# Kernel tuning notes

Measured on AMD Instinct MI355X. Metric: run time of the kernel, lower is better.

## Reference

```python
import jax, jax.numpy as jnp
import numpy as np
import math

B, S, DIM = 32, 1, 4096
NH, NKV, HD = 32, 8, 128
MAXLEN = 4096
START_POS = 4095


def _rope(t, freqs):
    # t: (b, s, h, hd); freqs: (s, hd//2, 2) = (cos/real, sin/imag)
    b, s, h, hd = t.shape
    tr = t.astype(jnp.float32).reshape(b, s, h, hd // 2, 2)
    c = freqs[None, :, None, :, 0]
    sn = freqs[None, :, None, :, 1]
    x0, x1 = tr[..., 0], tr[..., 1]
    out = jnp.stack([x0 * c - x1 * sn, x0 * sn + x1 * c], axis=-1)
    return out.reshape(b, s, h, hd).astype(t.dtype)


def setup_inputs() -> dict:
    key = jax.random.key(0)
    ks = jax.random.split(key, 8)
    sd = 1.0 / math.sqrt(DIM)
    x = jax.random.normal(ks[0], (B, S, DIM), dtype=jnp.float32)
    freqs = jax.random.normal(ks[1], (S, HD // 2, 2), dtype=jnp.float32)
    cache_k = jax.random.normal(ks[2], (B, MAXLEN, NKV, HD), dtype=jnp.float32)
    cache_v = jax.random.normal(ks[3], (B, MAXLEN, NKV, HD), dtype=jnp.float32)
    wq = jax.random.normal(ks[4], (NH * HD, DIM), dtype=jnp.float32) * sd
    wk = jax.random.normal(ks[5], (NKV * HD, DIM), dtype=jnp.float32) * sd
    wv = jax.random.normal(ks[6], (NKV * HD, DIM), dtype=jnp.float32) * sd
    wo = jax.random.normal(ks[7], (DIM, NH * HD), dtype=jnp.float32) * sd
    return {"x": x, "freqs": freqs, "cache_k": cache_k, "cache_v": cache_v,
            "wq": wq, "wk": wk, "wv": wv, "wo": wo, "start_pos": START_POS}


def reference(x, freqs, cache_k, cache_v, wq, wk, wv, wo, start_pos):
    b, s, _ = x.shape
    n_rep = NH // NKV
    xq = (x @ wq.T).reshape(b, s, NH, HD)
    xk = (x @ wk.T).reshape(b, s, NKV, HD)
    xv = (x @ wv.T).reshape(b, s, NKV, HD)
    xq = _rope(xq, freqs)
    xk = _rope(xk, freqs)
    # KV-cache write then read of prefix (static start_pos)
    keys = cache_k.at[:, start_pos:start_pos + s].set(xk)[:, :start_pos + s]
    values = cache_v.at[:, start_pos:start_pos + s].set(xv)[:, :start_pos + s]
    # GQA: group q heads (g=NKV kv groups, r=n_rep) without materializing repeat
    q = xq.reshape(b, s, NKV, n_rep, HD)
    scores = jnp.einsum('bsgrd,blgd->bgrsl', q, keys) / math.sqrt(HD)
    probs = jax.nn.softmax(scores.astype(jnp.float32), axis=-1).astype(xq.dtype)
    out = jnp.einsum('bgrsl,blgd->bsgrd', probs, values).reshape(b, s, NH * HD)
    return out @ wo.T
```

## Files before the change

kernel.cpp:

```cpp
#include <hip/hip_runtime.h>

#define QSCALE 0.08838834764831845f


#define GEMM_FMA(r, wf) \
    acc[r][0] = fmaf(wf.x, x0.x, acc[r][0]); acc[r][0] = fmaf(wf.y, x0.y, acc[r][0]); \
    acc[r][0] = fmaf(wf.z, x0.z, acc[r][0]); acc[r][0] = fmaf(wf.w, x0.w, acc[r][0]); \
    acc[r][1] = fmaf(wf.x, x1.x, acc[r][1]); acc[r][1] = fmaf(wf.y, x1.y, acc[r][1]); \
    acc[r][1] = fmaf(wf.z, x1.z, acc[r][1]); acc[r][1] = fmaf(wf.w, x1.w, acc[r][1]); \
    acc[r][2] = fmaf(wf.x, x2.x, acc[r][2]); acc[r][2] = fmaf(wf.y, x2.y, acc[r][2]); \
    acc[r][2] = fmaf(wf.z, x2.z, acc[r][2]); acc[r][2] = fmaf(wf.w, x2.w, acc[r][2]); \
    acc[r][3] = fmaf(wf.x, x3.x, acc[r][3]); acc[r][3] = fmaf(wf.y, x3.y, acc[r][3]); \
    acc[r][3] = fmaf(wf.z, x3.z, acc[r][3]); acc[r][3] = fmaf(wf.w, x3.w, acc[r][3]);

__device__ __forceinline__ void gemv3(
    const float* __restrict__ W,
    const float* __restrict__ X,
    float* __restrict__ part, const int M, const int m0, const int ks)
{
    const int t = threadIdx.x;
    const int ksub = t & 3;
    const int ngrp = (t >> 2) & 7;
    const int mgrp = t >> 5;

    const int kbase = ks * 256 + ksub * 4;
    const float* wr0 = W + (size_t)(mgrp * 8 + 0) * 4096 + kbase;
    const float* wr1 = W + (size_t)(mgrp * 8 + 1) * 4096 + kbase;
    const float* wr2 = W + (size_t)(mgrp * 8 + 2) * 4096 + kbase;
    const float* wr3 = W + (size_t)(mgrp * 8 + 3) * 4096 + kbase;
    const float* wr4 = W + (size_t)(mgrp * 8 + 4) * 4096 + kbase;
    const float* wr5 = W + (size_t)(mgrp * 8 + 5) * 4096 + kbase;
    const float* wr6 = W + (size_t)(mgrp * 8 + 6) * 4096 + kbase;
    const float* wr7 = W + (size_t)(mgrp * 8 + 7) * 4096 + kbase;
    const float* xr0 = X + (size_t)(ngrp * 4 + 0) * 4096 + kbase;
    const float* xr1 = X + (size_t)(ngrp * 4 + 1) * 4096 + kbase;
    const float* xr2 = X + (size_t)(ngrp * 4 + 2) * 4096 + kbase;
    const float* xr3 = X + (size_t)(ngrp * 4 + 3) * 4096 + kbase;

    float acc[8][4];
#pragma unroll
    for (int r = 0; r < 8; ++r)
#pragma unroll
        for (int n = 0; n < 4; ++n) acc[r][n] = 0.f;

#pragma unroll 2
    for (int c = 0; c < 16; ++c) {
        const int off = c * 16;
        const float4 w0 = *(const float4*)(wr0 + off);
        const float4 w1 = *(const float4*)(wr1 + off);
        const float4 w2 = *(const float4*)(wr2 + off);
        const float4 w3 = *(const float4*)(wr3 + off);
        const float4 w4 = *(const float4*)(wr4 + off);
        const float4 w5 = *(const float4*)(wr5 + off);
        const float4 w6 = *(const float4*)(wr6 + off);
        const float4 w7 = *(const float4*)(wr7 + off);
        const float4 x0 = *(const float4*)(xr0 + off);
        const float4 x1 = *(const float4*)(xr1 + off);
        const float4 x2 = *(const float4*)(xr2 + off);
        const float4 x3 = *(const float4*)(xr3 + off);
        GEMM_FMA(0, w0) GEMM_FMA(1, w1) GEMM_FMA(2, w2) GEMM_FMA(3, w3)
        GEMM_FMA(4, w4) GEMM_FMA(5, w5) GEMM_FMA(6, w6) GEMM_FMA(7, w7)
    }

#pragma unroll
    for (int r = 0; r < 8; ++r)
#pragma unroll
        for (int n = 0; n < 4; ++n) {
            acc[r][n] += __shfl_xor(acc[r][n], 1);
            acc[r][n] += __shfl_xor(acc[r][n], 2);
        }

    if (ksub == 0) {
        float* base = part + (size_t)ks * 32 * M + m0 + mgrp * 8;
#pragma unroll
        for (int n = 0; n < 4; ++n) {
            float* dst = base + (size_t)(ngrp * 4 + n) * M;
            *(float4*)(dst)     = make_float4(acc[0][n], acc[1][n], acc[2][n], acc[3][n]);
            *(float4*)(dst + 4) = make_float4(acc[4][n], acc[5][n], acc[6][n], acc[7][n]);
        }
    }
}

__global__ __launch_bounds__(256, 4) void gemv_qkv_kernel(
    const float* __restrict__ wq, const float* __restrict__ wk,
    const float* __restrict__ wv, const float* __restrict__ x,
    float* __restrict__ part)
{
    const int mb = blockIdx.x >> 4, ks = blockIdx.x & 15;
    const int m0 = mb * 64;
    const float* W;
    if (m0 < 4096)      W = wq + (size_t)m0 * 4096;
    else if (m0 < 5120) W = wk + (size_t)(m0 - 4096) * 4096;
    else                W = wv + (size_t)(m0 - 5120) * 4096;
    gemv3(W, x, part, 6144, m0, ks);
}

__global__ __launch_bounds__(256, 4) void gemv_out_kernel(
    const float* __restrict__ wo, const float* __restrict__ a_ws,
    float* __restrict__ part)
{
    const int mb = blockIdx.x >> 4, ks = blockIdx.x & 15;
    gemv3(wo + (size_t)(mb * 64) * 4096, a_ws, part, 4096, mb * 64, ks);
}

__global__ __launch_bounds__(256) void qkv_combine_kernel(
    const float* __restrict__ part,
    const float* __restrict__ freqs,
    float* __restrict__ qc_g, float* __restrict__ kn_g, float* __restrict__ vn_g)
{
    const int idx = blockIdx.x * 256 + threadIdx.x;
    const int b = idx / 1536;
    const int cm = (idx - b * 1536) * 4;
    const float* p = part + (size_t)b * 6144 + cm;
    float4 v = make_float4(0.f, 0.f, 0.f, 0.f);
#pragma unroll
    for (int s = 0; s < 16; ++s) {
        const float4 a = *(const float4*)(p + (size_t)s * (32 * 6144));
        v.x += a.x; v.y += a.y; v.z += a.z; v.w += a.w;
    }
    if (cm < 4096) {
        const int d = cm & 127;
        const float4 f = *(const float4*)(freqs + d);
        float4 o;
        o.x = (v.x * f.x - v.y * f.y) * QSCALE;
        o.y = (v.x * f.y + v.y * f.x) * QSCALE;
        o.z = (v.z * f.z - v.w * f.w) * QSCALE;
        o.w = (v.z * f.w + v.w * f.z) * QSCALE;
        *(float4*)(qc_g + (size_t)b * 4096 + cm) = o;
    } else if (cm < 5120) {
        const int d = (cm - 4096) & 127;
        const float4 f = *(const float4*)(freqs + d);
        float4 o;
        o.x = v.x * f.x - v.y * f.y;
        o.y = v.x * f.y + v.y * f.x;
        o.z = v.z * f.z - v.w * f.w;
        o.w = v.z * f.w + v.w * f.z;
        *(float4*)(kn_g + (size_t)b * 1024 + (cm - 4096)) = o;
    } else {
        *(float4*)(vn_g + (size_t)b * 1024 + (cm - 5120)) = v;
    }
}

__global__ __launch_bounds__(256, 4) void attn4_kernel(
    const float* __restrict__ qc_g, const float* __restrict__ kn_g,
    const float* __restrict__ vn_g,
    const float* __restrict__ cache_k, const float* __restrict__ cache_v,
    float* __restrict__ pmss, float* __restrict__ pacc)
{
    const int t = threadIdx.x;
    const int w = t >> 6, lane = t & 63;
    const int g2 = lane >> 5, j = lane & 31;
    const int bid = blockIdx.x;
    const int q2 = bid & 1, split = (bid >> 1) & 15, b = bid >> 5;
    const int gsub = w >> 1, rsub = w & 1;
    const int g = q2 * 4 + gsub * 2 + g2;
    const int row0 = split * 256 + rsub * 128;

    float4 q[4];
    const float* qb = qc_g + (size_t)b * 4096 + (size_t)g * 512 + j * 4;
#pragma unroll
    for (int h = 0; h < 4; ++h) q[h] = *(const float4*)(qb + h * 128);

    float m[4]  = {-1e30f, -1e30f, -1e30f, -1e30f};
    float ss[4] = {0.f, 0.f, 0.f, 0.f};
    float4 acc[4];
#pragma unroll
    for (int h = 0; h < 4; ++h) acc[h] = make_float4(0.f, 0.f, 0.f, 0.f);

    auto process = [&](const float4 kf, const float4 vf) {
        float d[4];
#pragma unroll
        for (int h = 0; h < 4; ++h)
            d[h] = fmaf(q[h].x, kf.x, fmaf(q[h].y, kf.y,
                   fmaf(q[h].z, kf.z, q[h].w * kf.w)));
#pragma unroll
        for (int mask = 1; mask <= 16; mask <<= 1) {
            d[0] += __shfl_xor(d[0], mask);
            d[1] += __shfl_xor(d[1], mask);
            d[2] += __shfl_xor(d[2], mask);
            d[3] += __shfl_xor(d[3], mask);
        }
#pragma unroll
        for (int h = 0; h < 4; ++h) {
            const float dd = d[h] - m[h];
            float pe;
            if (dd > 8.0f) {
                const float c = __expf(-dd);
                ss[h] = fmaf(ss[h], c, 1.0f);
                acc[h].x *= c; acc[h].y *= c; acc[h].z *= c; acc[h].w *= c;
                m[h] = d[h]; pe = 1.0f;
            } else {
                pe = __expf(dd);
                ss[h] += pe;
            }
            acc[h].x = fmaf(pe, vf.x, acc[h].x);
            acc[h].y = fmaf(pe, vf.y, acc[h].y);
            acc[h].z = fmaf(pe, vf.z, acc[h].z);
            acc[h].w = fmaf(pe, vf.w, acc[h].w);
        }
    };

    const size_t cbase = ((size_t)b * 4096 + row0) * 1024 + (size_t)g * 128 + j * 4;
    const float* kp = cache_k + cbase;
    const float* vp = cache_v + cbase;

    const bool lastw = (split == 15) && (rsub == 1);
    const int n = lastw ? 127 : 128;

    float4 kA = *(const float4*)(kp);
    float4 vA = *(const float4*)(vp);
    float4 kB = *(const float4*)(kp + 1024);
    float4 vB = *(const float4*)(vp + 1024);
#pragma unroll 2
    for (int i = 0; i < n; ++i) {
        float4 kC, vC;
        if (i + 2 < n) {
            kC = *(const float4*)(kp + (size_t)(i + 2) * 1024);
            vC = *(const float4*)(vp + (size_t)(i + 2) * 1024);
        }
        process(kA, vA);
        kA = kB; vA = vB; kB = kC; vB = vC;
    }
    if (lastw) {
        const float4 kf = *(const float4*)(kn_g + (size_t)b * 1024 + (size_t)g * 128 + j * 4);
        const float4 vf = *(const float4*)(vn_g + (size_t)b * 1024 + (size_t)g * 128 + j * 4);
        process(kf, vf);
    }

    const int pidx = (((b * 16 + split) * 2 + rsub) * 8 + g) * 4;
#pragma unroll
    for (int h = 0; h < 4; ++h)
        *(float4*)(pacc + (size_t)(pidx + h) * 128 + j * 4) = acc[h];
    if (j == 0) {
#pragma unroll
        for (int h = 0; h < 4; ++h) {
            pmss[(size_t)(pidx + h) * 2]     = m[h];
            pmss[(size_t)(pidx + h) * 2 + 1] = ss[h];
        }
    }
}

__global__ __launch_bounds__(128) void attn_combine_kernel(
    const float* __restrict__ pmss, const float* __restrict__ pacc,
    float* __restrict__ a_ws)
{
    const int bg = blockIdx.x, t = threadIdx.x;
    const int h = t >> 5, jj = t & 31;
    const int b = bg >> 3, g = bg & 7;

    float M = -1e30f;
#pragma unroll
    for (int s = 0; s < 16; ++s)
#pragma unroll
        for (int r = 0; r < 2; ++r) {
            const int idx = (((b * 16 + s) * 2 + r) * 8 + g) * 4 + h;
            M = fmaxf(M, pmss[(size_t)idx * 2]);
        }
    float SS = 0.f;
    float4 o = make_float4(0.f, 0.f, 0.f, 0.f);
#pragma unroll
    for (int s = 0; s < 16; ++s)
#pragma unroll
        for (int r = 0; r < 2; ++r) {
            const int idx = (((b * 16 + s) * 2 + r) * 8 + g) * 4 + h;
            const float wgt = __expf(pmss[(size_t)idx * 2] - M);
            SS = fmaf(pmss[(size_t)idx * 2 + 1], wgt, SS);
            const float4 a = *(const float4*)(pacc + (size_t)idx * 128 + jj * 4);
            o.x = fmaf(a.x, wgt, o.x);
            o.y = fmaf(a.y, wgt, o.y);
            o.z = fmaf(a.z, wgt, o.z);
            o.w = fmaf(a.w, wgt, o.w);
        }
    const float inv = 1.f / SS;
    o.x *= inv; o.y *= inv; o.z *= inv; o.w *= inv;
    *(float4*)(a_ws + (size_t)b * 4096 + (size_t)(g * 4 + h) * 128 + jj * 4) = o;
}

__global__ __launch_bounds__(256) void out_combine_kernel(
    const float* __restrict__ part, float* __restrict__ out)
{
    const int i4 = (blockIdx.x * 256 + threadIdx.x) * 4;
    float4 v = make_float4(0.f, 0.f, 0.f, 0.f);
#pragma unroll
    for (int s = 0; s < 16; ++s) {
        const float4 a = *(const float4*)(part + (size_t)s * 131072 + i4);
        v.x += a.x; v.y += a.y; v.z += a.z; v.w += a.w;
    }
    *(float4*)(out + i4) = v;
}

extern "C" void kernel_launch(void* const* d_in, const int* in_sizes, int n_in,
                              void* d_out, int out_size, void* d_ws, size_t ws_size,
                              hipStream_t stream)
{
    const float* x       = (const float*)d_in[0];
    const float* freqs   = (const float*)d_in[1];
    const float* cache_k = (const float*)d_in[2];
    const float* cache_v = (const float*)d_in[3];
    const float* wq      = (const float*)d_in[4];
    const float* wk      = (const float*)d_in[5];
    const float* wv      = (const float*)d_in[6];
    const float* wo      = (const float*)d_in[7];

    float* out = (float*)d_out;
    float* ws  = (float*)d_ws;
    float* part_qkv = ws;
    float* qc_g     = ws + 3145728;
    float* kn_g     = ws + 3276800;
    float* vn_g     = ws + 3309568;
    float* pmss     = ws + 3342336;
    float* pacc     = ws + 3407872;
    float* a_ws     = ws + 7602176;
    float* part_out = ws + 7733248;

    gemv_qkv_kernel<<<1536, 256, 0, stream>>>(wq, wk, wv, x, part_qkv);
    qkv_combine_kernel<<<192, 256, 0, stream>>>(part_qkv, freqs, qc_g, kn_g, vn_g);
    attn4_kernel<<<1024, 256, 0, stream>>>(qc_g, kn_g, vn_g, cache_k, cache_v, pmss, pacc);
    attn_combine_kernel<<<256, 128, 0, stream>>>(pmss, pacc, a_ws);
    gemv_out_kernel<<<1024, 256, 0, stream>>>(wo, a_ws, part_out);
    out_combine_kernel<<<128, 256, 0, stream>>>(part_out, out);
}
```

Before: 330.8 us.

## Fuse QKV split-K reduction and RoPE into attention kernel, deepen KV prefetch

Removes the separate qkv_combine kernel. Each attention block now reduces the 16 split-K partials for its own q heads and k/v group, applies RoPE and the q scaling, and stages the results in shared memory. This saves one launch and the round trip of q/k/v through global memory. The cost is redundant reduction work, because 16 splits per batch each recompute the same q/k/v. The KV loop is also restructured to prefetch four rows at a time instead of two, to keep more loads in flight.

```diff
diff --git a/kernel.cpp b/kernel.cpp
--- a/kernel.cpp
+++ b/kernel.cpp
@@ -103,47 +103,9 @@
     gemv3(wo + (size_t)(mb * 64) * 4096, a_ws, part, 4096, mb * 64, ks);
 }
 
-__global__ __launch_bounds__(256) void qkv_combine_kernel(
-    const float* __restrict__ part,
+__global__ __launch_bounds__(256, 4) void attn5_kernel(
+    const float* __restrict__ part_qkv,
     const float* __restrict__ freqs,
-    float* __restrict__ qc_g, float* __restrict__ kn_g, float* __restrict__ vn_g)
-{
-    const int idx = blockIdx.x * 256 + threadIdx.x;
-    const int b = idx / 1536;
-    const int cm = (idx - b * 1536) * 4;
-    const float* p = part + (size_t)b * 6144 + cm;
-    float4 v = make_float4(0.f, 0.f, 0.f, 0.f);
-#pragma unroll
-    for (int s = 0; s < 16; ++s) {
-        const float4 a = *(const float4*)(p + (size_t)s * (32 * 6144));
-        v.x += a.x; v.y += a.y; v.z += a.z; v.w += a.w;
-    }
-    if (cm < 4096) {
-        const int d = cm & 127;
-        const float4 f = *(const float4*)(freqs + d);
-        float4 o;
-        o.x = (v.x * f.x - v.y * f.y) * QSCALE;
-        o.y = (v.x * f.y + v.y * f.x) * QSCALE;
-        o.z = (v.z * f.z - v.w * f.w) * QSCALE;
-        o.w = (v.z * f.w + v.w * f.z) * QSCALE;
-        *(float4*)(qc_g + (size_t)b * 4096 + cm) = o;
-    } else if (cm < 5120) {
-        const int d = (cm - 4096) & 127;
-        const float4 f = *(const float4*)(freqs + d);
-        float4 o;
-        o.x = v.x * f.x - v.y * f.y;
-        o.y = v.x * f.y + v.y * f.x;
-        o.z = v.z * f.z - v.w * f.w;
-        o.w = v.z * f.w + v.w * f.z;
-        *(float4*)(kn_g + (size_t)b * 1024 + (cm - 4096)) = o;
-    } else {
-        *(float4*)(vn_g + (size_t)b * 1024 + (cm - 5120)) = v;
-    }
-}
-
-__global__ __launch_bounds__(256, 4) void attn4_kernel(
-    const float* __restrict__ qc_g, const float* __restrict__ kn_g,
-    const float* __restrict__ vn_g,
     const float* __restrict__ cache_k, const float* __restrict__ cache_v,
     float* __restrict__ pmss, float* __restrict__ pacc)
 {
@@ -153,13 +115,65 @@
     const int bid = blockIdx.x;
     const int q2 = bid & 1, split = (bid >> 1) & 15, b = bid >> 5;
     const int gsub = w >> 1, rsub = w & 1;
-    const int g = q2 * 4 + gsub * 2 + g2;
+    const int g  = q2 * 4 + gsub * 2 + g2;
+    const int gl = gsub * 2 + g2;
     const int row0 = split * 256 + rsub * 128;
 
+    __shared__ float qc[16][128];
+    __shared__ float knl[4][128];
+    __shared__ float vnl[4][128];
+
+    const size_t PS = 32 * 6144;
+    {
+        const int H = t >> 4, dq = (t & 15) * 8;
+        const float* p = part_qkv + (size_t)b * 6144 + (size_t)(q2 * 16 + H) * 128 + dq;
+        float4 s0 = make_float4(0.f, 0.f, 0.f, 0.f);
+        float4 s1 = make_float4(0.f, 0.f, 0.f, 0.f);
+#pragma unroll
+        for (int s = 0; s < 16; ++s) {
+            const float4 a = *(const float4*)(p + s * PS);
+            const float4 c = *(const float4*)(p + s * PS + 4);
+            s0.x += a.x; s0.y += a.y; s0.z += a.z; s0.w += a.w;
+            s1.x += c.x; s1.y += c.y; s1.z += c.z; s1.w += c.w;
+        }
+        const float4 f0 = *(const float4*)(freqs + dq);
+        const float4 f1 = *(const float4*)(freqs + dq + 4);
+        qc[H][dq + 0] = (s0.x * f0.x - s0.y * f0.y) * QSCALE;
+        qc[H][dq + 1] = (s0.x * f0.y + s0.y * f0.x) * QSCALE;
+        qc[H][dq + 2] = (s0.z * f0.z - s0.w * f0.w) * QSCALE;
+        qc[H][dq + 3] = (s0.z * f0.w + s0.w * f0.z) * QSCALE;
+        qc[H][dq + 4] = (s1.x * f1.x - s1.y * f1.y) * QSCALE;
+        qc[H][dq + 5] = (s1.x * f1.y + s1.y * f1.x) * QSCALE;
+        qc[H][dq + 6] = (s1.z * f1.z - s1.w * f1.w) * QSCALE;
+        qc[H][dq + 7] = (s1.z * f1.w + s1.w * f1.z) * QSCALE;
+    }
+    {
+        const int tv = t & 127;
+        const int glp = tv >> 5, d4 = (tv & 31) * 4;
+        const int moff = (t < 128 ? 4096 : 5120) + (q2 * 4 + glp) * 128 + d4;
+        const float* p = part_qkv + (size_t)b * 6144 + moff;
+        float4 s0 = make_float4(0.f, 0.f, 0.f, 0.f);
+#pragma unroll
+        for (int s = 0; s < 16; ++s) {
+            const float4 a = *(const float4*)(p + s * PS);
+            s0.x += a.x; s0.y += a.y; s0.z += a.z; s0.w += a.w;
+        }
+        if (t < 128) {
+            const float4 f = *(const float4*)(freqs + d4);
+            knl[glp][d4 + 0] = s0.x * f.x - s0.y * f.y;
+            knl[glp][d4 + 1] = s0.x * f.y + s0.y * f.x;
+            knl[glp][d4 + 2] = s0.z * f.z - s0.w * f.w;
+            knl[glp][d4 + 3] = s0.z * f.w + s0.w * f.z;
+        } else {
+            vnl[glp][d4 + 0] = s0.x; vnl[glp][d4 + 1] = s0.y;
+            vnl[glp][d4 + 2] = s0.z; vnl[glp][d4 + 3] = s0.w;
+        }
+    }
+    __syncthreads();
+
     float4 q[4];
-    const float* qb = qc_g + (size_t)b * 4096 + (size_t)g * 512 + j * 4;
-#pragma unroll
-    for (int h = 0; h < 4; ++h) q[h] = *(const float4*)(qb + h * 128);
+#pragma unroll
+    for (int h = 0; h < 4; ++h) q[h] = *(const float4*)&qc[gl * 4 + h][j * 4];
 
     float m[4]  = {-1e30f, -1e30f, -1e30f, -1e30f};
     float ss[4] = {0.f, 0.f, 0.f, 0.f};
@@ -207,23 +221,40 @@
     const bool lastw = (split == 15) && (rsub == 1);
     const int n = lastw ? 127 : 128;
 
-    float4 kA = *(const float4*)(kp);
-    float4 vA = *(const float4*)(vp);
-    float4 kB = *(const float4*)(kp + 1024);
-    float4 vB = *(const float4*)(vp + 1024);
-#pragma unroll 2
-    for (int i = 0; i < n; ++i) {
-        float4 kC, vC;
-        if (i + 2 < n) {
-            kC = *(const float4*)(kp + (size_t)(i + 2) * 1024);
-            vC = *(const float4*)(vp + (size_t)(i + 2) * 1024);
-        }
+    float4 kA, vA, kB, vB, kC, vC, kD, vD;
+    kA = *(const float4*)(kp);        vA = *(const float4*)(vp);
+    kB = *(const float4*)(kp + 1024); vB = *(const float4*)(vp + 1024);
+    int i = 0;
+    for (; i + 4 <= n; i += 4) {
+        const float* k2 = kp + (size_t)(i + 2) * 1024;
+        const float* v2 = vp + (size_t)(i + 2) * 1024;
+        kC = *(const float4*)(k2);        vC = *(const float4*)(v2);
+        kD = *(const float4*)(k2 + 1024); vD = *(const float4*)(v2 + 1024);
         process(kA, vA);
-        kA = kB; vA = vB; kB = kC; vB = vC;
+        process(kB, vB);
+        if (i + 6 <= n) {
+            const float* k4 = kp + (size_t)(i + 4) * 1024;
+            const float* v4 = vp + (size_t)(i + 4) * 1024;
+            kA = *(const float4*)(k4);        vA = *(const float4*)(v4);
+            kB = *(const float4*)(k4 + 1024); vB = *(const float4*)(v4 + 1024);
+        } else if (i + 5 <= n) {
+            const float* k4 = kp + (size_t)(i + 4) * 1024;
+            const float* v4 = vp + (size_t)(i + 4) * 1024;
+            kA = *(const float4*)(k4); vA = *(const float4*)(v4);
+        }
+        process(kC, vC);
+        process(kD, vD);
+    }
+    if (i < n)     process(kA, vA);
+    if (i + 1 < n) process(kB, vB);
+    if (i + 2 < n) {
+        const float4 kf = *(const float4*)(kp + (size_t)(i + 2) * 1024);
+        const float4 vf = *(const float4*)(vp + (size_t)(i + 2) * 1024);
+        process(kf, vf);
     }
     if (lastw) {
-        const float4 kf = *(const float4*)(kn_g + (size_t)b * 1024 + (size_t)g * 128 + j * 4);
-        const float4 vf = *(const float4*)(vn_g + (size_t)b * 1024 + (size_t)g * 128 + j * 4);
+        const float4 kf = *(const float4*)&knl[gl][j * 4];
+        const float4 vf = *(const float4*)&vnl[gl][j * 4];
         process(kf, vf);
     }
 
@@ -305,17 +336,13 @@
     float* out = (float*)d_out;
     float* ws  = (float*)d_ws;
     float* part_qkv = ws;
-    float* qc_g     = ws + 3145728;
-    float* kn_g     = ws + 3276800;
-    float* vn_g     = ws + 3309568;
-    float* pmss     = ws + 3342336;
-    float* pacc     = ws + 3407872;
-    float* a_ws     = ws + 7602176;
-    float* part_out = ws + 7733248;
+    float* pmss     = ws + 3145728;
+    float* pacc     = ws + 3211264;
+    float* a_ws     = ws + 7405568;
+    float* part_out = ws + 7536640;
 
     gemv_qkv_kernel<<<1536, 256, 0, stream>>>(wq, wk, wv, x, part_qkv);
-    qkv_combine_kernel<<<192, 256, 0, stream>>>(part_qkv, freqs, qc_g, kn_g, vn_g);
-    attn4_kernel<<<1024, 256, 0, stream>>>(qc_g, kn_g, vn_g, cache_k, cache_v, pmss, pacc);
+    attn5_kernel<<<1024, 256, 0, stream>>>(part_qkv, freqs, cache_k, cache_v, pmss, pacc);
     attn_combine_kernel<<<256, 128, 0, stream>>>(pmss, pacc, a_ws);
     gemv_out_kernel<<<1024, 256, 0, stream>>>(wo, a_ws, part_out);
     out_combine_kernel<<<128, 256, 0, stream>>>(part_out, out);
```

Result: slower. 346.3 us (+4.7%).

## Distribute per-head softmax state across lanes and deepen KV prefetch in attention

Applied to the files above, without the earlier changes.

The attention kernel now gives each lane one head's score after a transposed butterfly reduction. That replaces four per-head running max/sum states with a single scalar per lane and lowers register pressure so the occupancy bound can rise from 4 to 6. Rescaling now runs only when any lane sees the score jump by more than 8, and the exp and weight values are shared across lanes by shuffles. The KV loop prefetches four rows at a time instead of two. The trade-off is extra shuffles per key and new head/lane index remapping in the partial stores.

```diff
diff --git a/kernel.cpp b/kernel.cpp
--- a/kernel.cpp
+++ b/kernel.cpp
@@ -141,7 +141,7 @@
     }
 }
 
-__global__ __launch_bounds__(256, 4) void attn4_kernel(
+__global__ __launch_bounds__(256, 6) void attn6_kernel(
     const float* __restrict__ qc_g, const float* __restrict__ kn_g,
     const float* __restrict__ vn_g,
     const float* __restrict__ cache_k, const float* __restrict__ cache_v,
@@ -150,6 +150,7 @@
     const int t = threadIdx.x;
     const int w = t >> 6, lane = t & 63;
     const int g2 = lane >> 5, j = lane & 31;
+    const int o3 = j & 3;
     const int bid = blockIdx.x;
     const int q2 = bid & 1, split = (bid >> 1) & 15, b = bid >> 5;
     const int gsub = w >> 1, rsub = w & 1;
@@ -161,11 +162,10 @@
 #pragma unroll
     for (int h = 0; h < 4; ++h) q[h] = *(const float4*)(qb + h * 128);
 
-    float m[4]  = {-1e30f, -1e30f, -1e30f, -1e30f};
-    float ss[4] = {0.f, 0.f, 0.f, 0.f};
+    float m_s = -1e30f, ss_s = 0.f;
     float4 acc[4];
 #pragma unroll
-    for (int h = 0; h < 4; ++h) acc[h] = make_float4(0.f, 0.f, 0.f, 0.f);
+    for (int s = 0; s < 4; ++s) acc[s] = make_float4(0.f, 0.f, 0.f, 0.f);
 
     auto process = [&](const float4 kf, const float4 vf) {
         float d[4];
@@ -173,31 +173,41 @@
         for (int h = 0; h < 4; ++h)
             d[h] = fmaf(q[h].x, kf.x, fmaf(q[h].y, kf.y,
                    fmaf(q[h].z, kf.z, q[h].w * kf.w)));
-#pragma unroll
-        for (int mask = 1; mask <= 16; mask <<= 1) {
-            d[0] += __shfl_xor(d[0], mask);
-            d[1] += __shfl_xor(d[1], mask);
-            d[2] += __shfl_xor(d[2], mask);
-            d[3] += __shfl_xor(d[3], mask);
-        }
-#pragma unroll
-        for (int h = 0; h < 4; ++h) {
-            const float dd = d[h] - m[h];
-            float pe;
-            if (dd > 8.0f) {
-                const float c = __expf(-dd);
-                ss[h] = fmaf(ss[h], c, 1.0f);
-                acc[h].x *= c; acc[h].y *= c; acc[h].z *= c; acc[h].w *= c;
-                m[h] = d[h]; pe = 1.0f;
-            } else {
-                pe = __expf(dd);
-                ss[h] += pe;
-            }
-            acc[h].x = fmaf(pe, vf.x, acc[h].x);
-            acc[h].y = fmaf(pe, vf.y, acc[h].y);
-            acc[h].z = fmaf(pe, vf.z, acc[h].z);
-            acc[h].w = fmaf(pe, vf.w, acc[h].w);
-        }
+        d[0] += __shfl_xor(d[0], 1); d[1] += __shfl_xor(d[1], 1);
+        d[2] += __shfl_xor(d[2], 1); d[3] += __shfl_xor(d[3], 1);
+        d[0] += __shfl_xor(d[0], 2); d[1] += __shfl_xor(d[1], 2);
+        d[2] += __shfl_xor(d[2], 2); d[3] += __shfl_xor(d[3], 2);
+        const float t0 = (o3 & 1) ? d[1] : d[0];
+        const float t1 = (o3 & 1) ? d[3] : d[2];
+        float dsc = (o3 & 2) ? t1 : t0;
+        dsc += __shfl_xor(dsc, 4);
+        dsc += __shfl_xor(dsc, 8);
+        dsc += __shfl_xor(dsc, 16);
+        if (__any(dsc - m_s > 8.0f)) {
+            const float nm = fmaxf(m_s, dsc);
+            const float c  = __expf(m_s - nm);
+            m_s = nm; ss_s *= c;
+            const float c1 = __shfl_xor(c, 1);
+            const float c2 = __shfl_xor(c, 2);
+            const float c3 = __shfl_xor(c1, 2);
+            acc[0].x *= c;  acc[0].y *= c;  acc[0].z *= c;  acc[0].w *= c;
+            acc[1].x *= c1; acc[1].y *= c1; acc[1].z *= c1; acc[1].w *= c1;
+            acc[2].x *= c2; acc[2].y *= c2; acc[2].z *= c2; acc[2].w *= c2;
+            acc[3].x *= c3; acc[3].y *= c3; acc[3].z *= c3; acc[3].w *= c3;
+        }
+        const float pe = __expf(dsc - m_s);
+        ss_s += pe;
+        const float p1 = __shfl_xor(pe, 1);
+        const float p2 = __shfl_xor(pe, 2);
+        const float p3 = __shfl_xor(p1, 2);
+        acc[0].x = fmaf(pe, vf.x, acc[0].x); acc[0].y = fmaf(pe, vf.y, acc[0].y);
+        acc[0].z = fmaf(pe, vf.z, acc[0].z); acc[0].w = fmaf(pe, vf.w, acc[0].w);
+        acc[1].x = fmaf(p1, vf.x, acc[1].x); acc[1].y = fmaf(p1, vf.y, acc[1].y);
+        acc[1].z = fmaf(p1, vf.z, acc[1].z); acc[1].w = fmaf(p1, vf.w, acc[1].w);
+        acc[2].x = fmaf(p2, vf.x, acc[2].x); acc[2].y = fmaf(p2, vf.y, acc[2].y);
+        acc[2].z = fmaf(p2, vf.z, acc[2].z); acc[2].w = fmaf(p2, vf.w, acc[2].w);
+        acc[3].x = fmaf(p3, vf.x, acc[3].x); acc[3].y = fmaf(p3, vf.y, acc[3].y);
+        acc[3].z = fmaf(p3, vf.z, acc[3].z); acc[3].w = fmaf(p3, vf.w, acc[3].w);
     };
 
     const size_t cbase = ((size_t)b * 4096 + row0) * 1024 + (size_t)g * 128 + j * 4;
@@ -207,19 +217,36 @@
     const bool lastw = (split == 15) && (rsub == 1);
     const int n = lastw ? 127 : 128;
 
-    float4 kA = *(const float4*)(kp);
-    float4 vA = *(const float4*)(vp);
-    float4 kB = *(const float4*)(kp + 1024);
-    float4 vB = *(const float4*)(vp + 1024);
-#pragma unroll 2
-    for (int i = 0; i < n; ++i) {
-        float4 kC, vC;
-        if (i + 2 < n) {
-            kC = *(const float4*)(kp + (size_t)(i + 2) * 1024);
-            vC = *(const float4*)(vp + (size_t)(i + 2) * 1024);
-        }
+    float4 kA, vA, kB, vB, kC, vC, kD, vD;
+    kA = *(const float4*)(kp);        vA = *(const float4*)(vp);
+    kB = *(const float4*)(kp + 1024); vB = *(const float4*)(vp + 1024);
+    int i = 0;
+    for (; i + 4 <= n; i += 4) {
+        const float* k2 = kp + (size_t)(i + 2) * 1024;
+        const float* v2 = vp + (size_t)(i + 2) * 1024;
+        kC = *(const float4*)(k2);        vC = *(const float4*)(v2);
+        kD = *(const float4*)(k2 + 1024); vD = *(const float4*)(v2 + 1024);
         process(kA, vA);
-        kA = kB; vA = vB; kB = kC; vB = vC;
+        process(kB, vB);
+        if (i + 6 <= n) {
+            const float* k4 = kp + (size_t)(i + 4) * 1024;
+            const float* v4 = vp + (size_t)(i + 4) * 1024;
+            kA = *(const float4*)(k4);        vA = *(const float4*)(v4);
+            kB = *(const float4*)(k4 + 1024); vB = *(const float4*)(v4 + 1024);
+        } else if (i + 5 <= n) {
+            const float* k4 = kp + (size_t)(i + 4) * 1024;
+            const float* v4 = vp + (size_t)(i + 4) * 1024;
+            kA = *(const float4*)(k4); vA = *(const float4*)(v4);
+        }
+        process(kC, vC);
+        process(kD, vD);
+    }
+    if (i < n)     process(kA, vA);
+    if (i + 1 < n) process(kB, vB);
+    if (i + 2 < n) {
+        const float4 kf = *(const float4*)(kp + (size_t)(i + 2) * 1024);
+        const float4 vf = *(const float4*)(vp + (size_t)(i + 2) * 1024);
+        process(kf, vf);
     }
     if (lastw) {
         const float4 kf = *(const float4*)(kn_g + (size_t)b * 1024 + (size_t)g * 128 + j * 4);
@@ -229,14 +256,13 @@
 
     const int pidx = (((b * 16 + split) * 2 + rsub) * 8 + g) * 4;
 #pragma unroll
-    for (int h = 0; h < 4; ++h)
-        *(float4*)(pacc + (size_t)(pidx + h) * 128 + j * 4) = acc[h];
-    if (j == 0) {
-#pragma unroll
-        for (int h = 0; h < 4; ++h) {
-            pmss[(size_t)(pidx + h) * 2]     = m[h];
-            pmss[(size_t)(pidx + h) * 2 + 1] = ss[h];
-        }
+    for (int s = 0; s < 4; ++s) {
+        const int head = o3 ^ s;
+        *(float4*)(pacc + (size_t)(pidx + head) * 128 + j * 4) = acc[s];
+    }
+    if (j < 4) {
+        pmss[(size_t)(pidx + j) * 2]     = m_s;
+        pmss[(size_t)(pidx + j) * 2 + 1] = ss_s;
     }
 }
 
@@ -273,7 +299,7 @@
         }
     const float inv = 1.f / SS;
     o.x *= inv; o.y *= inv; o.z *= inv; o.w *= inv;
-    *(float4*)(a_ws + (size_t)b * 4096 + (size_t)(g * 4 + h) * 128 + jj * 4) = o;
+    *(float4*)&a_ws[(size_t)b * 4096 + (size_t)(g * 4 + h) * 128 + jj * 4] = o;
 }
 
 __global__ __launch_bounds__(256) void out_combine_kernel(
@@ -315,7 +341,7 @@
 
     gemv_qkv_kernel<<<1536, 256, 0, stream>>>(wq, wk, wv, x, part_qkv);
     qkv_combine_kernel<<<192, 256, 0, stream>>>(part_qkv, freqs, qc_g, kn_g, vn_g);
-    attn4_kernel<<<1024, 256, 0, stream>>>(qc_g, kn_g, vn_g, cache_k, cache_v, pmss, pacc);
+    attn6_kernel<<<1024, 256, 0, stream>>>(qc_g, kn_g, vn_g, cache_k, cache_v, pmss, pacc);
     attn_combine_kernel<<<256, 128, 0, stream>>>(pmss, pacc, a_ws);
     gemv_out_kernel<<<1024, 256, 0, stream>>>(wo, a_ws, part_out);
     out_combine_kernel<<<128, 256, 0, stream>>>(part_out, out);
```

New measurement: 443.8 us. 1.34x slower.
